# Kernel tuning notes

Hardware: AMD Instinct MI355X
Metric: run time of the kernel (lower is better)

The kernel has to match this reference:

```python
import jax, jax.numpy as jnp
import numpy as np

EPS = 1e-5
NUM_HEADS = 16

def rmsnorm(x, w=None, eps=EPS):
    y = x * jax.lax.rsqrt(jnp.mean(x * x, axis=-1, keepdims=True) + eps)
    return y if w is None else y * w

def act_quant(x):
    # per-token 8-bit absmax activation quantization (BitNet b1.58)
    scale = 127.0 / jnp.clip(jnp.max(jnp.abs(x), axis=-1, keepdims=True), 1e-5, None)
    return jnp.clip(jnp.round(x * scale), -128, 127) / scale

def weight_quant(w):
    # ternary (1.58-bit) absmean weight quantization
    scale = 1.0 / jnp.clip(jnp.mean(jnp.abs(w)), 1e-5, None)
    return jnp.clip(jnp.round(w * scale), -1, 1) / scale

def bit_linear(x, w):
    # BitLinear: RMSNorm -> STE-quantized activation @ STE-quantized ternary weight
    xn = rmsnorm(x)
    xq = xn + jax.lax.stop_gradient(act_quant(xn) - xn)
    wq = w + jax.lax.stop_gradient(weight_quant(w) - w)
    return xq @ wq.T

def hgrn_recurrence(i, logf):
    # elementwise gated linear recurrence: h_t = exp(logf_t) * h_{t-1} + i_t
    def step(h, xs):
        ii, ff = xs
        h = jnp.exp(ff) * h + ii
        return h, h
    B, T, D = i.shape
    _, o = jax.lax.scan(step, jnp.zeros((B, D), i.dtype),
                        (jnp.swapaxes(i, 0, 1), jnp.swapaxes(logf, 0, 1)))
    return jnp.swapaxes(o, 0, 1)  # [B, T, D]

def hgrn_bit_attention(x, w_i, w_f, w_g, w_o, g_norm_w):
    i = bit_linear(x, w_i)
    f = bit_linear(x, w_f)
    logf = jax.nn.log_sigmoid(f)
    i = jax.nn.silu(i) * (1.0 - jax.nn.sigmoid(f))  # swiglu(i, 1 - sigmoid(f))
    o = hgrn_recurrence(i, logf)
    g = bit_linear(x, w_g)
    B, T, D = o.shape
    oh = rmsnorm(o.reshape(B, T, NUM_HEADS, D // NUM_HEADS), g_norm_w)  # per-head RMSNorm
    o = oh.reshape(B, T, D) * g * jax.nn.sigmoid(g)  # swish gate (FusedRMSNormSwishGate)
    return bit_linear(o, w_o)

def setup_inputs() -> dict:
    key = jax.random.key(0)
    B, S_S, S_C, D = 4, 4096, 512, 2048
    ks = jax.random.split(key, 16)
    mk = lambda k: jax.random.normal(k, (D, D), jnp.float32) * 0.02
    return {
        "hidden_states": jax.random.normal(ks[0], (B, S_S, D), jnp.float32),
        "encoder_hidden_states": jax.random.normal(ks[1], (B, S_C, D), jnp.float32),
        "w_q": mk(ks[2]), "w_k": mk(ks[3]), "w_v": mk(ks[4]), "w_out": mk(ks[5]),
        "w_add_q": mk(ks[6]), "w_add_k": mk(ks[7]), "w_add_v": mk(ks[8]), "w_add_out": mk(ks[9]),
        "w_i": mk(ks[10]), "w_f": mk(ks[11]), "w_g": mk(ks[12]), "w_o": mk(ks[13]),
        "g_norm_w": jnp.ones((D // NUM_HEADS,), jnp.float32),
    }

def reference(hidden_states, encoder_hidden_states, w_q, w_k, w_v, w_out,
              w_add_q, w_add_k, w_add_v, w_add_out, w_i, w_f, w_g, w_o, g_norm_w):
    q_s = bit_linear(hidden_states, w_q)
    k_s = bit_linear(hidden_states, w_k)          # computed as in original; unused by attn
    v_s = bit_linear(hidden_states, w_v)          # computed as in original; unused by attn
    q_c = bit_linear(encoder_hidden_states, w_add_q)
    k_c = bit_linear(encoder_hidden_states, w_add_k)
    v_c = bit_linear(encoder_hidden_states, w_add_v)
    q_joint = jnp.concatenate([q_c, q_s], axis=1)  # context first, then stream
    attn_out = hgrn_bit_attention(q_joint, w_i, w_f, w_g, w_o, g_norm_w)
    len_c = encoder_hidden_states.shape[1]
    out_c, out_s = attn_out[:, :len_c, :], attn_out[:, len_c:, :]
    return (bit_linear(out_s, w_out), bit_linear(out_c, w_add_out))
```

## Files before the change

### kernel.cpp

```cpp
#include <hip/hip_runtime.h>
#include <math.h>
#include <stdint.h>

#define D2 2048

typedef int v4i __attribute__((ext_vector_type(4)));
typedef int v16i __attribute__((ext_vector_type(16)));
typedef float v4f __attribute__((ext_vector_type(4)));

struct Ptrs8 { const float* p[8]; };
struct RowMap { int seg, jump, off; };

enum { QW_Q = 0, QW_OUT = 1, QW_ADDQ = 2, QW_ADDOUT = 3, QW_I = 4, QW_F = 5, QW_G = 6, QW_O = 7 };

__device__ __forceinline__ int rmap(RowMap m, int r) {
  return (r / m.seg) * m.jump + (r % m.seg) + m.off;
}

__device__ __forceinline__ void gload16(const void* g, void* l) {
  __builtin_amdgcn_global_load_lds((__attribute__((address_space(1))) void*)g,
                                   (__attribute__((address_space(3))) void*)l, 16, 0, 0);
}

__device__ __forceinline__ float fsig(float x) {
  return __builtin_amdgcn_rcpf(1.0f + __expf(-x));
}

template <bool NT>
__device__ __forceinline__ void stf(float* p, float v) {
  if (NT) __builtin_nontemporal_store(v, p);
  else *p = v;
}

__device__ __forceinline__ v4f ldnt4(const float* p) {
  return __builtin_nontemporal_load((const v4f*)p);
}

__device__ __forceinline__ int swz(int r) { return ((r >> 1) & 3) ^ ((r >> 3) & 3); }

__device__ __forceinline__ void gswz16(int nM, int& mb, int& nb) {
  int bid = blockIdx.x;
  int wg = (bid & 7) * (nM << 1) + (bid >> 3);
  mb = wg >> 4;
  nb = wg & 15;
}
__device__ __forceinline__ void gswz8(int nM, int& mb, int& nb) {
  int bid = blockIdx.x;
  int wg = (bid & 7) * nM + (bid >> 3);
  mb = wg >> 3;
  nb = wg & 7;
}

__global__ __launch_bounds__(256) void k_wabs(Ptrs8 wsrc, double* part) {
  int m = blockIdx.y;
  const float* w0 = wsrc.p[m] + (size_t)blockIdx.x * 4096 + threadIdx.x * 16;
  double s = 0.0;
#pragma unroll
  for (int j = 0; j < 4; ++j) {
    v4f v = ldnt4(w0 + j * 4);
    s += (double)fabsf(v[0]) + (double)fabsf(v[1]) + (double)fabsf(v[2]) + (double)fabsf(v[3]);
  }
#pragma unroll
  for (int o = 32; o; o >>= 1) s += __shfl_down(s, o);
  __shared__ double red[4];
  if ((threadIdx.x & 63) == 0) red[threadIdx.x >> 6] = s;
  __syncthreads();
  if (threadIdx.x == 0) part[(size_t)m * 1024 + blockIdx.x] = red[0] + red[1] + red[2] + red[3];
}

__global__ __launch_bounds__(256) void k_wmean(const double* part, double* wqs, float* wmul) {
  int m = blockIdx.x, t = threadIdx.x;
  const double* p = part + (size_t)m * 1024;
  double s = p[t] + p[t + 256] + p[t + 512] + p[t + 768];
#pragma unroll
  for (int o = 32; o; o >>= 1) s += __shfl_down(s, o);
  __shared__ double red[4];
  if ((t & 63) == 0) red[t >> 6] = s;
  __syncthreads();
  if (t == 0) {
    double mean = (red[0] + red[1] + red[2] + red[3]) * (1.0 / 4194304.0);
    double cl = mean > 1e-5 ? mean : 1e-5;
    wqs[m] = 1.0 / cl;
    wmul[m] = (float)cl;
  }
}

__global__ __launch_bounds__(256) void k_wquant(Ptrs8 wsrc, const double* wqs, int8_t* wq) {
  int m = blockIdx.y;
  double qs = wqs[m];
  size_t base = (size_t)blockIdx.x * 4096 + threadIdx.x * 16;
  const float* w0 = wsrc.p[m] + base;
  union { int8_t b[16]; int4 v; } u;
#pragma unroll
  for (int j = 0; j < 4; ++j) {
    v4f v = ldnt4(w0 + j * 4);
#pragma unroll
    for (int c = 0; c < 4; ++c) {
      int q = (int)rint((double)v[c] * qs);
      q = q > 1 ? 1 : (q < -1 ? -1 : q);
      u.b[j * 4 + c] = (int8_t)q;
    }
  }
  *(int4*)(wq + (size_t)m * 4194304 + base) = u.v;
}

__global__ __launch_bounds__(256) void k_actq(const float* __restrict__ x, int8_t* __restrict__ q,
                                              float* __restrict__ inv) {
  int row = blockIdx.x, t = threadIdx.x;
  const float* xr = x + (size_t)row * D2 + (size_t)t * 8;
  v4f a = ldnt4(xr);
  v4f b = ldnt4(xr + 4);
  float v[8] = {a[0], a[1], a[2], a[3], b[0], b[1], b[2], b[3]};
  float ss = 0.f, ma = 0.f;
#pragma unroll
  for (int j = 0; j < 8; ++j) { ss += v[j] * v[j]; ma = fmaxf(ma, fabsf(v[j])); }
#pragma unroll
  for (int o = 32; o; o >>= 1) { ss += __shfl_down(ss, o); ma = fmaxf(ma, __shfl_down(ma, o)); }
  __shared__ float rs[4], rm[4], bc[2];
  if ((t & 63) == 0) { rs[t >> 6] = ss; rm[t >> 6] = ma; }
  __syncthreads();
  if (t == 0) {
    float S = rs[0] + rs[1] + rs[2] + rs[3];
    float M = fmaxf(fmaxf(rm[0], rm[1]), fmaxf(rm[2], rm[3]));
    float r = 1.0f / sqrtf(S * (1.0f / 2048.0f) + 1e-5f);
    float mx = fmaxf(M * r, 1e-5f);
    bc[0] = r;
    bc[1] = 127.0f / mx;
    inv[row] = mx * (1.0f / 127.0f);
  }
  __syncthreads();
  float r = bc[0], s = bc[1];
  union { int8_t b8[8]; int2 p2; } u;
#pragma unroll
  for (int j = 0; j < 8; ++j) {
    float xn = v[j] * r;
    int qq = (int)rintf(xn * s);
    qq = qq > 127 ? 127 : (qq < -128 ? -128 : qq);
    u.b8[j] = (int8_t)qq;
  }
  ((int2*)(q + (size_t)row * D2))[t] = u.p2;
}

#define SYNC_PIPE(N)                                          \
  do {                                                        \
    __builtin_amdgcn_sched_barrier(0);                        \
    asm volatile("s_waitcnt vmcnt(" #N ")" ::: "memory");     \
    __builtin_amdgcn_sched_barrier(0);                        \
    __builtin_amdgcn_s_barrier();                             \
    __builtin_amdgcn_sched_barrier(0);                        \
  } while (0)

__device__ __forceinline__ void gemm_mainloop(const int8_t* __restrict__ Aq,
                                              const int8_t* __restrict__ Wq, int ga0, int ga1,
                                              int n0, int t, int8_t* lds, v16i acc[2][4]) {
  const int wid = t >> 6, lane = t & 63;
  const int wr = wid >> 1, wc = wid & 1, am = lane & 31, g = lane >> 5;
  const int arow = t >> 2;
  const int achk = ((t & 3) ^ swz(arow)) * 16;
  const int8_t* agp0 = Aq + (size_t)ga0 * 2048 + achk;
  const int8_t* agp1 = Aq + (size_t)ga1 * 2048 + achk;
  const int8_t* bgp0 = Wq + (size_t)(n0 + arow) * 2048 + achk;
  const int8_t* bgp1 = Wq + (size_t)(n0 + 64 + arow) * 2048 + achk;
  const int8_t* bgp2 = Wq + (size_t)(n0 + 128 + arow) * 2048 + achk;
  const int8_t* bgp3 = Wq + (size_t)(n0 + 192 + arow) * 2048 + achk;

#define STAGEW(B)                                                \
  do {                                                           \
    gload16(agp0, lds + (B) + wid * 1024);                       \
    gload16(agp1, lds + (B) + 4096 + wid * 1024);                \
    gload16(bgp0, lds + (B) + 8192 + wid * 1024);                \
    gload16(bgp1, lds + (B) + 12288 + wid * 1024);               \
    gload16(bgp2, lds + (B) + 16384 + wid * 1024);               \
    gload16(bgp3, lds + (B) + 20480 + wid * 1024);               \
    agp0 += 64; agp1 += 64;                                      \
    bgp0 += 64; bgp1 += 64; bgp2 += 64; bgp3 += 64;              \
  } while (0)

#define COMPUTEW(B)                                                                         \
  do {                                                                                      \
    _Pragma("unroll") for (int kk = 0; kk < 2; ++kk) {                                      \
      v4i af[2], bf[4];                                                                     \
      _Pragma("unroll") for (int mi = 0; mi < 2; ++mi) {                                    \
        int r = wr * 64 + mi * 32 + am;                                                     \
        int slot = ((kk << 1) | g) ^ swz(r);                                                \
        af[mi] = *(const v4i*)(lds + (B) + r * 64 + slot * 16);                             \
      }                                                                                     \
      _Pragma("unroll") for (int ni = 0; ni < 4; ++ni) {                                    \
        int rb = wc * 128 + ni * 32 + am;                                                   \
        int slotb = ((kk << 1) | g) ^ swz(rb);                                              \
        bf[ni] = *(const v4i*)(lds + (B) + 8192 + rb * 64 + slotb * 16);                    \
      }                                                                                     \
      _Pragma("unroll") for (int mi = 0; mi < 2; ++mi)                                      \
        _Pragma("unroll") for (int ni = 0; ni < 4; ++ni)                                    \
          acc[mi][ni] =                                                                     \
              __builtin_amdgcn_mfma_i32_32x32x32_i8(af[mi], bf[ni], acc[mi][ni], 0, 0, 0);  \
    }                                                                                       \
  } while (0)

  STAGEW(0);
  STAGEW(24576);
  STAGEW(49152);
  SYNC_PIPE(12);
#pragma unroll 1
  for (int tt = 0; tt < 30; tt += 3) {
    COMPUTEW(0);
    SYNC_PIPE(6);
    if (tt + 3 < 32) STAGEW(0);
    COMPUTEW(24576);
    SYNC_PIPE(6);
    if (tt + 4 < 32) STAGEW(24576);
    COMPUTEW(49152);
    SYNC_PIPE(6);
    if (tt + 5 < 32) STAGEW(49152);
  }
  COMPUTEW(0);
  SYNC_PIPE(0);
  COMPUTEW(24576);
#undef STAGEW
#undef COMPUTEW
}

template <bool NT>
__device__ __forceinline__ void gemm_body(const int8_t* Aq, const float* ainv, const int8_t* Wq,
                                          const float* wmul, int widx, float* C, RowMap inm,
                                          RowMap outm, int m0, int n0, int t, int8_t* lds) {
  int lane = t & 63, wid = t >> 6;
  int wr = wid >> 1, wc = wid & 1;
  int am = lane & 31, g = lane >> 5;
  int ga0 = rmap(inm, m0 + (t >> 2));
  int ga1 = rmap(inm, m0 + 64 + (t >> 2));

  v16i acc[2][4] = {};
  gemm_mainloop(Aq, Wq, ga0, ga1, n0, t, lds, acc);

  float wm = wmul[widx];
#pragma unroll
  for (int mi = 0; mi < 2; ++mi) {
#pragma unroll
    for (int q = 0; q < 16; ++q) {
      int rin = wr * 64 + mi * 32 + (q & 3) + ((q >> 2) * 8) + g * 4;
      int ra = rmap(inm, m0 + rin);
      int rc = rmap(outm, m0 + rin);
      float s = ainv[ra] * wm;
#pragma unroll
      for (int ni = 0; ni < 4; ++ni) {
        stf<NT>(&C[(size_t)rc * 2048 + n0 + wc * 128 + ni * 32 + am], (float)acc[mi][ni][q] * s);
      }
    }
  }
}

template <bool NT>
__global__ __launch_bounds__(256) void k_gemm(const int8_t* __restrict__ Aq,
                                              const float* __restrict__ ainv,
                                              const int8_t* __restrict__ Wq,
                                              const float* __restrict__ wmul, int widx,
                                              float* __restrict__ C, RowMap inm, RowMap outm,
                                              int nM) {
  __shared__ __align__(16) int8_t lds[73728];
  int mb, nb;
  gswz8(nM, mb, nb);
  gemm_body<NT>(Aq, ainv, Wq, wmul, widx, C, inm, outm, mb * 128, nb * 256, threadIdx.x, lds);
}

template <bool NT>
__global__ __launch_bounds__(256) void k_gemm2(const int8_t* __restrict__ Aq,
                                               const float* __restrict__ ainv,
                                               const int8_t* __restrict__ W0, int w0idx,
                                               RowMap inm0, RowMap outm0, float* __restrict__ C0,
                                               int nM0,
                                               const int8_t* __restrict__ W1, int w1idx,
                                               RowMap inm1, RowMap outm1, float* __restrict__ C1,
                                               int nM1, const float* __restrict__ wmul) {
  __shared__ __align__(16) int8_t lds[73728];
  int mb, nb;
  gswz8(nM0 + nM1, mb, nb);
  if (mb < nM0) {
    gemm_body<NT>(Aq, ainv, W0, wmul, w0idx, C0, inm0, outm0, mb * 128, nb * 256, threadIdx.x,
                  lds);
  } else {
    gemm_body<NT>(Aq, ainv, W1, wmul, w1idx, C1, inm1, outm1, (mb - nM0) * 128, nb * 256,
                  threadIdx.x, lds);
  }
}

__global__ __launch_bounds__(256) void k_gemm_if(const int8_t* __restrict__ Aq,
                                                 const float* __restrict__ ainv,
                                                 const int8_t* __restrict__ Wi,
                                                 const int8_t* __restrict__ Wf,
                                                 const float* __restrict__ wmul,
                                                 float* __restrict__ IG, float* __restrict__ AD,
                                                 float* __restrict__ chA, float* __restrict__ chH,
                                                 int nM) {
  __shared__ __align__(16) int8_t lds[73728];
  int mb, nb;
  gswz16(nM, mb, nb);
  int m0 = mb * 128, n0 = nb * 128;
  int t = threadIdx.x;
  const int wid = t >> 6, lane = t & 63;
  const int wr = wid >> 1, wc = wid & 1, am = lane & 31, g = lane >> 5;
  const int arow = t >> 2;
  const int achk = ((t & 3) ^ swz(arow)) * 16;
  const int8_t* agp0 = Aq + (size_t)(m0 + arow) * 2048 + achk;
  const int8_t* agp1 = Aq + (size_t)(m0 + 64 + arow) * 2048 + achk;
  const int8_t* bip0 = Wi + (size_t)(n0 + arow) * 2048 + achk;
  const int8_t* bip1 = Wi + (size_t)(n0 + 64 + arow) * 2048 + achk;
  const int8_t* bfp0 = Wf + (size_t)(n0 + arow) * 2048 + achk;
  const int8_t* bfp1 = Wf + (size_t)(n0 + 64 + arow) * 2048 + achk;

  v16i acci[2][2] = {};
  v16i accf[2][2] = {};

#define STAGE_IF(B)                                                                   \
  do {                                                                                \
    gload16(agp0, lds + (B) + wid * 1024);                                            \
    gload16(agp1, lds + (B) + 4096 + wid * 1024);                                     \
    gload16(bip0, lds + (B) + 8192 + wid * 1024);                                     \
    gload16(bip1, lds + (B) + 12288 + wid * 1024);                                    \
    gload16(bfp0, lds + (B) + 16384 + wid * 1024);                                    \
    gload16(bfp1, lds + (B) + 20480 + wid * 1024);                                    \
    agp0 += 64; agp1 += 64; bip0 += 64; bip1 += 64; bfp0 += 64; bfp1 += 64;           \
  } while (0)

#define COMPUTE_IF(B)                                                                       \
  do {                                                                                      \
    _Pragma("unroll") for (int kk = 0; kk < 2; ++kk) {                                      \
      v4i af[2], bfi[2], bff[2];                                                            \
      _Pragma("unroll") for (int mi = 0; mi < 2; ++mi) {                                    \
        int r = wr * 64 + mi * 32 + am;                                                     \
        int slot = ((kk << 1) | g) ^ swz(r);                                                \
        af[mi] = *(const v4i*)(lds + (B) + r * 64 + slot * 16);                             \
      }                                                                                     \
      _Pragma("unroll") for (int ni = 0; ni < 2; ++ni) {                                    \
        int rb = wc * 64 + ni * 32 + am;                                                    \
        int slotb = ((kk << 1) | g) ^ swz(rb);                                              \
        bfi[ni] = *(const v4i*)(lds + (B) + 8192 + rb * 64 + slotb * 16);                   \
        bff[ni] = *(const v4i*)(lds + (B) + 16384 + rb * 64 + slotb * 16);                  \
      }                                                                                     \
      _Pragma("unroll") for (int mi = 0; mi < 2; ++mi)                                      \
        _Pragma("unroll") for (int ni = 0; ni < 2; ++ni) {                                  \
          acci[mi][ni] =                                                                    \
              __builtin_amdgcn_mfma_i32_32x32x32_i8(af[mi], bfi[ni], acci[mi][ni], 0, 0, 0);\
          accf[mi][ni] =                                                                    \
              __builtin_amdgcn_mfma_i32_32x32x32_i8(af[mi], bff[ni], accf[mi][ni], 0, 0, 0);\
        }                                                                                   \
    }                                                                                       \
  } while (0)

  STAGE_IF(0);
  STAGE_IF(24576);
  STAGE_IF(49152);
  SYNC_PIPE(12);
#pragma unroll 1
  for (int tt = 0; tt < 30; tt += 3) {
    COMPUTE_IF(0);
    SYNC_PIPE(6);
    if (tt + 3 < 32) STAGE_IF(0);
    COMPUTE_IF(24576);
    SYNC_PIPE(6);
    if (tt + 4 < 32) STAGE_IF(24576);
    COMPUTE_IF(49152);
    SYNC_PIPE(6);
    if (tt + 5 < 32) STAGE_IF(49152);
  }
  COMPUTE_IF(0);
  SYNC_PIPE(0);
  COMPUTE_IF(24576);
#undef STAGE_IF
#undef COMPUTE_IF

  float wmi = wmul[QW_I], wmf = wmul[QW_F];
  __syncthreads();
  float2* seglds = (float2*)lds;
#pragma unroll
  for (int mi = 0; mi < 2; ++mi) {
#pragma unroll
    for (int qh = 0; qh < 4; ++qh) {
      float segP[2], segH[2];
#pragma unroll
      for (int ql = 0; ql < 4; ++ql) {
        int q = qh * 4 + ql;
        int rloc = wr * 64 + mi * 32 + qh * 8 + g * 4 + ql;
        int rin = m0 + rloc;
        float ai = ainv[rin];
        float si = ai * wmi, sf = ai * wmf;
#pragma unroll
        for (int ni = 0; ni < 2; ++ni) {
          size_t idx = (size_t)rin * 2048 + n0 + wc * 64 + ni * 32 + am;
          float iv = (float)acci[mi][ni][q] * si;
          float fv = (float)accf[mi][ni][q] * sf;
          float a = fsig(fv);
          float s2 = iv * fsig(iv);
          float igv = s2 * (1.0f - a);
          __builtin_nontemporal_store(igv, &IG[idx]);
          __builtin_nontemporal_store(a, &AD[idx]);
          if (ql == 0) {
            segP[ni] = a;
            segH[ni] = igv;
          } else {
            segH[ni] = a * segH[ni] + igv;
            segP[ni] *= a;
          }
        }
      }
      int seg = wr * 16 + mi * 8 + qh * 2 + g;
#pragma unroll
      for (int ni = 0; ni < 2; ++ni)
        seglds[seg * 128 + wc * 64 + ni * 32 + am] = make_float2(segP[ni], segH[ni]);
    }
  }
  __syncthreads();
  if (t < 128) {
    float P = 1.f, H = 0.f;
#pragma unroll 1
    for (int s = 0; s < 32; ++s) {
      float2 e = seglds[s * 128 + t];
      H = e.x * H + e.y;
      P *= e.x;
    }
    int bb = mb / 36, ck = mb - bb * 36;
    int chain = bb * 2048 + n0 + t;
    chA[(size_t)ck * 8192 + chain] = P;
    chH[(size_t)ck * 8192 + chain] = H;
  }
}

__global__ __launch_bounds__(256) void k_rec2(const float* __restrict__ chA,
                                              const float* __restrict__ chH,
                                              float* __restrict__ chC) {
  int chain = blockIdx.x * 256 + threadIdx.x;
  float carry = 0.f;
  for (int c = 0; c < 36; ++c) {
    chC[(size_t)c * 8192 + chain] = carry;
    carry = chA[(size_t)c * 8192 + chain] * carry + chH[(size_t)c * 8192 + chain];
  }
}

__global__ __launch_bounds__(256) void k_rec3(float* __restrict__ io, const float* __restrict__ ad,
                                              const float* __restrict__ chC) {
  int tid = blockIdx.x * 256 + threadIdx.x;
  int chain = tid & 8191;
  int c = tid >> 13;
  int b = chain >> 11, d = chain & 2047;
  size_t base = ((size_t)b * 4608 + (size_t)c * 128) * 2048 + d;
  float h = chC[(size_t)c * 8192 + chain];
  for (int s = 0; s < 128; ++s) {
    float av = __builtin_nontemporal_load(ad + base);
    float iv = io[base];
    h = av * h + iv;
    io[base] = h;
    base += 2048;
  }
}

__global__ __launch_bounds__(256) void k_hnq(const float* __restrict__ o,
                                             const float* __restrict__ g,
                                             const float* __restrict__ gnw,
                                             int8_t* __restrict__ q, float* __restrict__ inv) {
  int row = blockIdx.x, t = threadIdx.x;
  size_t base = (size_t)row * D2 + (size_t)t * 8;
  v4f a = ldnt4(o + base);
  v4f b = ldnt4(o + base + 4);
  float v[8] = {a[0], a[1], a[2], a[3], b[0], b[1], b[2], b[3]};
  float ss = 0.f;
#pragma unroll
  for (int j = 0; j < 8; ++j) ss += v[j] * v[j];
  ss += __shfl_xor(ss, 1);
  ss += __shfl_xor(ss, 2);
  ss += __shfl_xor(ss, 4);
  ss += __shfl_xor(ss, 8);
  float r = 1.0f / sqrtf(ss * (1.0f / 128.0f) + 1e-5f);
  v4f ga = ldnt4(g + base);
  v4f gb = ldnt4(g + base + 4);
  float gv[8] = {ga[0], ga[1], ga[2], ga[3], gb[0], gb[1], gb[2], gb[3]};
  int j0 = (t & 15) * 8;
  float o2[8];
#pragma unroll
  for (int j = 0; j < 8; ++j) {
    float gg = gv[j];
    o2[j] = v[j] * r * gnw[j0 + j] * gg * fsig(gg);
  }
  float ss2 = 0.f, ma = 0.f;
#pragma unroll
  for (int j = 0; j < 8; ++j) { ss2 += o2[j] * o2[j]; ma = fmaxf(ma, fabsf(o2[j])); }
#pragma unroll
  for (int off = 32; off; off >>= 1) {
    ss2 += __shfl_down(ss2, off);
    ma = fmaxf(ma, __shfl_down(ma, off));
  }
  __shared__ float rs[4], rm[4], bc[2];
  if ((t & 63) == 0) { rs[t >> 6] = ss2; rm[t >> 6] = ma; }
  __syncthreads();
  if (t == 0) {
    float S = rs[0] + rs[1] + rs[2] + rs[3];
    float M = fmaxf(fmaxf(rm[0], rm[1]), fmaxf(rm[2], rm[3]));
    float rr = 1.0f / sqrtf(S * (1.0f / 2048.0f) + 1e-5f);
    float mx = fmaxf(M * rr, 1e-5f);
    bc[0] = rr;
    bc[1] = 127.0f / mx;
    inv[row] = mx * (1.0f / 127.0f);
  }
  __syncthreads();
  float rr = bc[0], s = bc[1];
  union { int8_t b8[8]; int2 p2; } u;
#pragma unroll
  for (int j = 0; j < 8; ++j) {
    float xn = o2[j] * rr;
    int qq = (int)rintf(xn * s);
    qq = qq > 127 ? 127 : (qq < -128 ? -128 : qq);
    u.b8[j] = (int8_t)qq;
  }
  ((int2*)(q + (size_t)row * D2))[t] = u.p2;
}

extern "C" void kernel_launch(void* const* d_in, const int* in_sizes, int n_in,
                              void* d_out, int out_size, void* d_ws, size_t ws_size,
                              hipStream_t stream) {
  const float* hid = (const float*)d_in[0];
  const float* enc = (const float*)d_in[1];
  const float* gnw = (const float*)d_in[14];
  Ptrs8 wp;
  wp.p[QW_Q] = (const float*)d_in[2];
  wp.p[QW_OUT] = (const float*)d_in[5];
  wp.p[QW_ADDQ] = (const float*)d_in[6];
  wp.p[QW_ADDOUT] = (const float*)d_in[9];
  wp.p[QW_I] = (const float*)d_in[10];
  wp.p[QW_F] = (const float*)d_in[11];
  wp.p[QW_G] = (const float*)d_in[12];
  wp.p[QW_O] = (const float*)d_in[13];
  float* out = (float*)d_out;

  char* ws = (char*)d_ws;
  float* bufA = (float*)ws;
  float* bufB = bufA + 37748736;
  int8_t* actq = (int8_t*)(bufB + 37748736);
  int8_t* wq = actq + 37748736;
  float* ainv = (float*)(wq + 33554432);
  double* wpart = (double*)(ainv + 18432);
  double* wqs = wpart + 8192;
  float* wmul = (float*)(wqs + 8);
  float* chA = wmul + 8;
  float* chH = chA + 524288;
  float* chC = chH + 524288;
  if (ws_size < 379723872ULL) return;

  RowMap idm{0x40000000, 0, 0};
  RowMap encoff{0x40000000, 0, 16384};
  RowMap seqm{4096, 4608, 512};
  RowMap encm{512, 4608, 0};

  k_wabs<<<dim3(1024, 8), 256, 0, stream>>>(wp, wpart);
  k_wmean<<<8, 256, 0, stream>>>(wpart, wqs, wmul);
  k_wquant<<<dim3(1024, 8), 256, 0, stream>>>(wp, wqs, wq);
  k_actq<<<16384, 256, 0, stream>>>(hid, actq, ainv);
  k_actq<<<2048, 256, 0, stream>>>(enc, actq + (size_t)16384 * 2048, ainv + 16384);
  k_gemm2<false><<<(128 + 16) * 8, 256, 0, stream>>>(
      actq, ainv, wq + (size_t)QW_Q * 4194304, QW_Q, idm, seqm, bufA, 128,
      wq + (size_t)QW_ADDQ * 4194304, QW_ADDQ, encoff, encm, bufA, 16, wmul);
  k_actq<<<18432, 256, 0, stream>>>(bufA, actq, ainv);
  k_gemm_if<<<144 * 16, 256, 0, stream>>>(actq, ainv, wq + (size_t)QW_I * 4194304,
                                          wq + (size_t)QW_F * 4194304, wmul, bufA, bufB,
                                          chA, chH, 144);
  k_gemm<true><<<144 * 8, 256, 0, stream>>>(actq, ainv, wq + (size_t)QW_G * 4194304, wmul,
                                            QW_G, out, idm, idm, 144);
  k_rec2<<<32, 256, 0, stream>>>(chA, chH, chC);
  k_rec3<<<1152, 256, 0, stream>>>(bufA, bufB, chC);
  k_hnq<<<18432, 256, 0, stream>>>(bufA, out, gnw, actq, ainv);
  k_gemm<false><<<144 * 8, 256, 0, stream>>>(actq, ainv, wq + (size_t)QW_O * 4194304, wmul,
                                             QW_O, bufB, idm, idm, 144);
  k_actq<<<18432, 256, 0, stream>>>(bufB, actq, ainv);
  k_gemm2<true><<<(128 + 16) * 8, 256, 0, stream>>>(
      actq, ainv, wq + (size_t)QW_OUT * 4194304, QW_OUT, seqm, idm, out, 128,
      wq + (size_t)QW_ADDOUT * 4194304, QW_ADDOUT, encm, idm, out + (size_t)33554432, 16, wmul);
}
```

Measured before the change: 920.7 us.

## Fuse recurrence carry application with head RMSNorm, swish gate and quantization

The chunk-local scan in the i/f GEMM epilogue now emits summaries for 64-row chunks instead of 128-row ones, doubling the chunk count to 72. The carry scan writes its carries in place over chA. A new fused kernel, k_rechq, replaces k_rec3 and k_hnq: it applies the carries, runs the recurrence row by row, and performs per-head RMSNorm, swish gating and int8 quantization without writing h back to memory. This removes a full read-write pass over the recurrence output, but each block now needs two __syncthreads per row and there are only 288 blocks of 1024 threads, so parallelism and latency hiding are reduced.

```diff
diff --git a/kernel.cpp b/kernel.cpp
--- a/kernel.cpp
+++ b/kernel.cpp
@@ -7,6 +7,7 @@
 typedef int v4i __attribute__((ext_vector_type(4)));
 typedef int v16i __attribute__((ext_vector_type(16)));
 typedef float v4f __attribute__((ext_vector_type(4)));
+typedef float v2f __attribute__((ext_vector_type(2)));
 
 struct Ptrs8 { const float* p[8]; };
 struct RowMap { int seg, jump, off; };
@@ -34,6 +35,9 @@
 
 __device__ __forceinline__ v4f ldnt4(const float* p) {
   return __builtin_nontemporal_load((const v4f*)p);
+}
+__device__ __forceinline__ v2f ldnt2(const float* p) {
+  return __builtin_nontemporal_load((const v2f*)p);
 }
 
 __device__ __forceinline__ int swz(int r) { return ((r >> 1) & 3) ^ ((r >> 3) & 3); }
@@ -411,106 +415,109 @@
   }
   __syncthreads();
   if (t < 128) {
-    float P = 1.f, H = 0.f;
+    int bb = mb / 36, lt = mb - bb * 36;
+    int chain = bb * 2048 + n0 + t;
+#pragma unroll
+    for (int half = 0; half < 2; ++half) {
+      float P = 1.f, H = 0.f;
 #pragma unroll 1
-    for (int s = 0; s < 32; ++s) {
-      float2 e = seglds[s * 128 + t];
-      H = e.x * H + e.y;
-      P *= e.x;
-    }
-    int bb = mb / 36, ck = mb - bb * 36;
-    int chain = bb * 2048 + n0 + t;
-    chA[(size_t)ck * 8192 + chain] = P;
-    chH[(size_t)ck * 8192 + chain] = H;
-  }
-}
-
-__global__ __launch_bounds__(256) void k_rec2(const float* __restrict__ chA,
-                                              const float* __restrict__ chH,
-                                              float* __restrict__ chC) {
+      for (int s = 0; s < 16; ++s) {
+        float2 e = seglds[(half * 16 + s) * 128 + t];
+        H = e.x * H + e.y;
+        P *= e.x;
+      }
+      int ck = lt * 2 + half;
+      chA[(size_t)ck * 8192 + chain] = P;
+      chH[(size_t)ck * 8192 + chain] = H;
+    }
+  }
+}
+
+__global__ __launch_bounds__(256) void k_rec2(float* __restrict__ chA,
+                                              const float* __restrict__ chH) {
   int chain = blockIdx.x * 256 + threadIdx.x;
   float carry = 0.f;
-  for (int c = 0; c < 36; ++c) {
-    chC[(size_t)c * 8192 + chain] = carry;
-    carry = chA[(size_t)c * 8192 + chain] * carry + chH[(size_t)c * 8192 + chain];
-  }
-}
-
-__global__ __launch_bounds__(256) void k_rec3(float* __restrict__ io, const float* __restrict__ ad,
-                                              const float* __restrict__ chC) {
-  int tid = blockIdx.x * 256 + threadIdx.x;
-  int chain = tid & 8191;
-  int c = tid >> 13;
-  int b = chain >> 11, d = chain & 2047;
-  size_t base = ((size_t)b * 4608 + (size_t)c * 128) * 2048 + d;
-  float h = chC[(size_t)c * 8192 + chain];
-  for (int s = 0; s < 128; ++s) {
-    float av = __builtin_nontemporal_load(ad + base);
-    float iv = io[base];
-    h = av * h + iv;
-    io[base] = h;
-    base += 2048;
-  }
-}
-
-__global__ __launch_bounds__(256) void k_hnq(const float* __restrict__ o,
-                                             const float* __restrict__ g,
-                                             const float* __restrict__ gnw,
-                                             int8_t* __restrict__ q, float* __restrict__ inv) {
-  int row = blockIdx.x, t = threadIdx.x;
-  size_t base = (size_t)row * D2 + (size_t)t * 8;
-  v4f a = ldnt4(o + base);
-  v4f b = ldnt4(o + base + 4);
-  float v[8] = {a[0], a[1], a[2], a[3], b[0], b[1], b[2], b[3]};
-  float ss = 0.f;
-#pragma unroll
-  for (int j = 0; j < 8; ++j) ss += v[j] * v[j];
-  ss += __shfl_xor(ss, 1);
-  ss += __shfl_xor(ss, 2);
-  ss += __shfl_xor(ss, 4);
-  ss += __shfl_xor(ss, 8);
-  float r = 1.0f / sqrtf(ss * (1.0f / 128.0f) + 1e-5f);
-  v4f ga = ldnt4(g + base);
-  v4f gb = ldnt4(g + base + 4);
-  float gv[8] = {ga[0], ga[1], ga[2], ga[3], gb[0], gb[1], gb[2], gb[3]};
-  int j0 = (t & 15) * 8;
-  float o2[8];
-#pragma unroll
-  for (int j = 0; j < 8; ++j) {
-    float gg = gv[j];
-    o2[j] = v[j] * r * gnw[j0 + j] * gg * fsig(gg);
-  }
-  float ss2 = 0.f, ma = 0.f;
-#pragma unroll
-  for (int j = 0; j < 8; ++j) { ss2 += o2[j] * o2[j]; ma = fmaxf(ma, fabsf(o2[j])); }
-#pragma unroll
-  for (int off = 32; off; off >>= 1) {
-    ss2 += __shfl_down(ss2, off);
-    ma = fmaxf(ma, __shfl_down(ma, off));
-  }
-  __shared__ float rs[4], rm[4], bc[2];
-  if ((t & 63) == 0) { rs[t >> 6] = ss2; rm[t >> 6] = ma; }
-  __syncthreads();
-  if (t == 0) {
-    float S = rs[0] + rs[1] + rs[2] + rs[3];
-    float M = fmaxf(fmaxf(rm[0], rm[1]), fmaxf(rm[2], rm[3]));
-    float rr = 1.0f / sqrtf(S * (1.0f / 2048.0f) + 1e-5f);
-    float mx = fmaxf(M * rr, 1e-5f);
-    bc[0] = rr;
-    bc[1] = 127.0f / mx;
-    inv[row] = mx * (1.0f / 127.0f);
-  }
-  __syncthreads();
-  float rr = bc[0], s = bc[1];
-  union { int8_t b8[8]; int2 p2; } u;
-#pragma unroll
-  for (int j = 0; j < 8; ++j) {
-    float xn = o2[j] * rr;
-    int qq = (int)rintf(xn * s);
-    qq = qq > 127 ? 127 : (qq < -128 ? -128 : qq);
-    u.b8[j] = (int8_t)qq;
-  }
-  ((int2*)(q + (size_t)row * D2))[t] = u.p2;
+  for (int c = 0; c < 72; ++c) {
+    size_t ix = (size_t)c * 8192 + chain;
+    float a = chA[ix];
+    float h = chH[ix];
+    chA[ix] = carry;
+    carry = a * carry + h;
+  }
+}
+
+__global__ __launch_bounds__(1024) void k_rechq(const float* __restrict__ ig,
+                                                const float* __restrict__ ad,
+                                                const float* __restrict__ carry,
+                                                const float* __restrict__ g,
+                                                const float* __restrict__ gnw,
+                                                int8_t* __restrict__ q,
+                                                float* __restrict__ inv) {
+  int blk = blockIdx.x;
+  int b = blk / 72, c = blk - b * 72;
+  int t = threadIdx.x;
+  int col = t * 2;
+  int wave = t >> 6;
+  int gr0 = b * 4608 + c * 64;
+  size_t base = (size_t)gr0 * 2048 + col;
+  float h0 = carry[(size_t)c * 8192 + b * 2048 + col];
+  float h1 = carry[(size_t)c * 8192 + b * 2048 + col + 1];
+  float w0 = gnw[col & 127];
+  float w1 = gnw[(col & 127) + 1];
+  __shared__ float redS[16], redM[16], bcv[2];
+
+  v2f igc = ldnt2(ig + base);
+  v2f adc = ldnt2(ad + base);
+  v2f gc = ldnt2(g + base);
+#pragma unroll 1
+  for (int s = 0; s < 64; ++s) {
+    size_t nbase = base + 2048;
+    v2f ign, adn, gn;
+    if (s < 63) {
+      ign = ldnt2(ig + nbase);
+      adn = ldnt2(ad + nbase);
+      gn = ldnt2(g + nbase);
+    }
+    h0 = adc[0] * h0 + igc[0];
+    h1 = adc[1] * h1 + igc[1];
+    float sh = h0 * h0 + h1 * h1;
+#pragma unroll
+    for (int o = 32; o; o >>= 1) sh += __shfl_xor(sh, o);
+    float r = 1.0f / sqrtf(sh * (1.0f / 128.0f) + 1e-5f);
+    float o20 = h0 * r * w0 * gc[0] * fsig(gc[0]);
+    float o21 = h1 * r * w1 * gc[1] * fsig(gc[1]);
+    float ss2 = o20 * o20 + o21 * o21;
+    float mx = fmaxf(fabsf(o20), fabsf(o21));
+#pragma unroll
+    for (int o = 32; o; o >>= 1) {
+      ss2 += __shfl_xor(ss2, o);
+      mx = fmaxf(mx, __shfl_xor(mx, o));
+    }
+    if ((t & 63) == 0) { redS[wave] = ss2; redM[wave] = mx; }
+    __syncthreads();
+    if (t == 0) {
+      float S = 0.f, M = 0.f;
+#pragma unroll
+      for (int wv = 0; wv < 16; ++wv) { S += redS[wv]; M = fmaxf(M, redM[wv]); }
+      float rr = 1.0f / sqrtf(S * (1.0f / 2048.0f) + 1e-5f);
+      float mxr = fmaxf(M * rr, 1e-5f);
+      bcv[0] = rr;
+      bcv[1] = 127.0f / mxr;
+      inv[gr0 + s] = mxr * (1.0f / 127.0f);
+    }
+    __syncthreads();
+    float rr = bcv[0], sc = bcv[1];
+    int q0 = (int)rintf(o20 * rr * sc);
+    int q1 = (int)rintf(o21 * rr * sc);
+    q0 = q0 > 127 ? 127 : (q0 < -128 ? -128 : q0);
+    q1 = q1 > 127 ? 127 : (q1 < -128 ? -128 : q1);
+    unsigned short pk = (unsigned short)(((q1 & 0xff) << 8) | (q0 & 0xff));
+    *(unsigned short*)(q + (size_t)(gr0 + s) * 2048 + col) = pk;
+    base = nbase;
+    igc = ign;
+    adc = adn;
+    gc = gn;
+  }
 }
 
 extern "C" void kernel_launch(void* const* d_in, const int* in_sizes, int n_in,
@@ -540,8 +547,7 @@
   double* wqs = wpart + 8192;
   float* wmul = (float*)(wqs + 8);
   float* chA = wmul + 8;
-  float* chH = chA + 524288;
-  float* chC = chH + 524288;
+  float* chH = chA + 589824;
   if (ws_size < 379723872ULL) return;
 
   RowMap idm{0x40000000, 0, 0};
@@ -563,9 +569,8 @@
                                           chA, chH, 144);
   k_gemm<true><<<144 * 8, 256, 0, stream>>>(actq, ainv, wq + (size_t)QW_G * 4194304, wmul,
                                             QW_G, out, idm, idm, 144);
-  k_rec2<<<32, 256, 0, stream>>>(chA, chH, chC);
-  k_rec3<<<1152, 256, 0, stream>>>(bufA, bufB, chC);
-  k_hnq<<<18432, 256, 0, stream>>>(bufA, out, gnw, actq, ainv);
+  k_rec2<<<32, 256, 0, stream>>>(chA, chH);
+  k_rechq<<<288, 1024, 0, stream>>>(bufA, bufB, chA, out, gnw, actq, ainv);
   k_gemm<false><<<144 * 8, 256, 0, stream>>>(actq, ainv, wq + (size_t)QW_O * 4194304, wmul,
                                              QW_O, bufB, idm, idm, 144);
   k_actq<<<18432, 256, 0, stream>>>(bufB, actq, ainv);
```

Measured after the change: 948.2 us. 1.03x slower.
